# Kernel optimization log

Measured on AMD Instinct MI355X. Metric: run time of the kernel, lower is better.

Reference implementation:

```python
import jax, jax.numpy as jnp
import numpy as np

NEG_BIG = -9e15
LRELU_SLOPE = 0.2  # alpha

N = 8192
IN_F = 256
OUT_F = 128


def setup_inputs() -> dict:
    key = jax.random.key(0)
    k1, k2, k3, k4 = jax.random.split(key, 4)
    inputs = jax.random.normal(k1, (N, IN_F), dtype=jnp.float32)
    adj = jax.random.randint(k2, (N, N), 0, 2, dtype=jnp.int32)
    # xavier_uniform with gain=1.414
    gain = 1.414
    bW = gain * np.sqrt(6.0 / (IN_F + OUT_F))
    W = jax.random.uniform(k3, (IN_F, OUT_F), minval=-bW, maxval=bW, dtype=jnp.float32)
    ba = gain * np.sqrt(6.0 / (2 * OUT_F + 1))
    a = jax.random.uniform(k4, (2 * OUT_F, 1), minval=-ba, maxval=ba, dtype=jnp.float32)
    return {"inputs": inputs, "adj": adj, "W": W, "a": a}


def reference(inputs, adj, W, a):
    # h: [N, F']
    h = inputs @ W
    # a^T [h_i || h_j] = h_i . a[:F'] + h_j . a[F':]  -- avoids the O(N^2 * 2F') concat
    a1 = a[:OUT_F, 0]   # [F']
    a2 = a[OUT_F:, 0]   # [F']
    s1 = h @ a1         # [N]
    s2 = h @ a2         # [N]
    e = s1[:, None] + s2[None, :]                      # [N, N]
    e = jnp.where(e >= 0, e, LRELU_SLOPE * e)          # LeakyReLU(alpha)
    scores = jnp.where(adj > 0, e, jnp.float32(NEG_BIG))
    attention = jax.nn.softmax(scores, axis=1)         # row softmax; dropout p=0
    h_prime = attention @ h                            # [N, F']
    return jax.nn.elu(h_prime)                         # concat=True -> elu
```

## Files before the change

### kernel.cpp

```cpp
#include <hip/hip_runtime.h>
#include <hip/hip_bf16.h>

#define NN   8192
#define INF_ 256
#define OUTF 128
#define SLOPE 0.2f
#define NCH  2
#define CHJ  1024
#define NT_  16
#define NP_  16

typedef float f32x4  __attribute__((ext_vector_type(4)));
typedef float f32x16 __attribute__((ext_vector_type(16)));
typedef short bf16x8 __attribute__((ext_vector_type(8)));
typedef int   i32x4  __attribute__((ext_vector_type(4)));
typedef unsigned int u32;
typedef unsigned short u16;
typedef u16 u16x2 __attribute__((ext_vector_type(2)));

__device__ __forceinline__ u16 f2bf(float f) {
  return __builtin_bit_cast(u16, __float2bfloat16(f));
}


__global__ __launch_bounds__(256) void gat_k1(
    const float* __restrict__ X, const float* __restrict__ W,
    const float* __restrict__ a, u16* __restrict__ hbF,
    float* __restrict__ s1, float* __restrict__ s2) {
  __shared__ float xs[16 * INF_];
  const int t = threadIdx.x;
  const int r0 = blockIdx.x * 16;
  {
    const f32x4* src = (const f32x4*)(X + (size_t)r0 * INF_);
    f32x4* dst = (f32x4*)xs;
#pragma unroll
    for (int i = 0; i < 4; i++) dst[t + 256 * i] = src[t + 256 * i];
  }
  __syncthreads();
  const int cg = t & 31;
  const int rg = t >> 5;
  float acc[2][4];
#pragma unroll
  for (int i = 0; i < 2; i++)
#pragma unroll
    for (int j = 0; j < 4; j++) acc[i][j] = 0.f;

  for (int k = 0; k < INF_; k += 4) {
    f32x4 xv[2];
#pragma unroll
    for (int i = 0; i < 2; i++) xv[i] = *(const f32x4*)&xs[(rg * 2 + i) * INF_ + k];
#pragma unroll
    for (int kk = 0; kk < 4; kk++) {
      f32x4 wv = *(const f32x4*)&W[(k + kk) * OUTF + cg * 4];
#pragma unroll
      for (int i = 0; i < 2; i++)
#pragma unroll
        for (int j = 0; j < 4; j++) acc[i][j] = fmaf(xv[i][kk], wv[j], acc[i][j]);
    }
  }

  f32x4 a1v = *(const f32x4*)&a[cg * 4];
  f32x4 a2v = *(const f32x4*)&a[OUTF + cg * 4];
  float p1[2], p2[2];
#pragma unroll
  for (int i = 0; i < 2; i++) {
    p1[i] = acc[i][0] * a1v[0] + acc[i][1] * a1v[1] + acc[i][2] * a1v[2] + acc[i][3] * a1v[3];
    p2[i] = acc[i][0] * a2v[0] + acc[i][1] * a2v[1] + acc[i][2] * a2v[2] + acc[i][3] * a2v[3];
  }
#pragma unroll
  for (int m = 1; m < 32; m <<= 1) {
#pragma unroll
    for (int i = 0; i < 2; i++) {
      p1[i] += __shfl_xor(p1[i], m);
      p2[i] += __shfl_xor(p2[i], m);
    }
  }
  if (cg == 0) {
#pragma unroll
    for (int i = 0; i < 2; i++) {
      s1[r0 + rg * 2 + i] = p1[i];
      s2[r0 + rg * 2 + i] = p2[i];
    }
  }

  const int R0 = r0 + rg * 2;
  const int cc = R0 >> 10;
  const int rest = R0 & 1023;
  const int pr = rest >> 7;
  const int tt = (rest >> 3) & 15;
  const int e0 = R0 & 7;
  const int w_ = pr >> 1;
  const int g_ = pr & 1;
  const int n  = (cc * 16 + tt) * 4 + w_;
#pragma unroll
  for (int j = 0; j < 4; j++) {
    const int C = cg * 4 + j;
    u16x2 pk = {f2bf(acc[0][j]), f2bf(acc[1][j])};
    *(u16x2*)(hbF + ((size_t)(n * 4 + (C >> 5)) * 64 + g_ * 32 + (C & 31)) * 8 + e0) = pk;
  }
}

__global__ __launch_bounds__(256) void gat_k2(const float* __restrict__ s2,
                                              float* __restrict__ bmax,
                                              float* __restrict__ E1,
                                              float* __restrict__ E2) {
  __shared__ float sm[4];
  const int t = threadIdx.x;
  const int i = blockIdx.x * 256 + t;
  f32x4 v = ((const f32x4*)s2)[i];
  f32x4 e1, e2;
  float m = -1e30f;
#pragma unroll
  for (int k = 0; k < 4; k++) {
    m = fmaxf(m, v[k]);
    e1[k] = __expf(v[k]);
    e2[k] = __expf(SLOPE * v[k]);
  }
  ((f32x4*)E1)[i] = e1;
  ((f32x4*)E2)[i] = e2;
#pragma unroll
  for (int k = 1; k < 64; k <<= 1) m = fmaxf(m, __shfl_xor(m, k));
  if ((t & 63) == 0) sm[t >> 6] = m;
  __syncthreads();
  if (t == 0)
    bmax[blockIdx.x] = fmaxf(fmaxf(sm[0], sm[1]), fmaxf(sm[2], sm[3]));
}

__device__ __forceinline__ void st16(float* dst, const f32x16& A, int g) {
#pragma unroll
  for (int r = 0; r < 16; r++) {
    const int dr = (r & 3) + 8 * (r >> 2) + 4 * g;
    dst[dr * 128] = A[r];
  }
}
__device__ __forceinline__ void ad16(float* dst, const f32x16& A, int g) {
#pragma unroll
  for (int r = 0; r < 16; r++) {
    const int dr = (r & 3) + 8 * (r >> 2) + 4 * g;
    dst[dr * 128] += A[r];
  }
}

__global__ __launch_bounds__(256, 4) void gat_k3(
    const int* __restrict__ adj, const u16* __restrict__ hbF,
    const float* __restrict__ s1g, const float* __restrict__ E1,
    const float* __restrict__ E2, const float* __restrict__ bmax,
    float* __restrict__ part, float* __restrict__ dpart) {
  __shared__ unsigned char mb[2][4096];
  __shared__ float lred[4096];
  __shared__ float dred[128];
  const int t = threadIdx.x;
  const int w = t >> 6;
  const int l = t & 63;
  const int rb = blockIdx.x >> 2;
  const int jq = blockIdx.x & 3;
  const int r0 = rb * 32;
  const int row = l & 31;
  const int g = l >> 5;
  const int pr = 2 * w + g;

  float s2m = bmax[0];
#pragma unroll
  for (int k = 1; k < 8; k++) s2m = fmaxf(s2m, bmax[k]);
  const float s1r = s1g[r0 + row];
  float Mi = s1r + s2m;
  Mi = fmaxf(Mi, SLOPE * Mi);
  const float A = __expf(s1r - Mi);
  const float B = __expf(SLOPE * s1r - Mi);

  const int srow = t >> 3;
  const int cl = t & 7;
  const int* gsrc = adj + (size_t)(r0 + srow) * NN + jq * (NCH * CHJ) + cl * 8;

  i32x4 sA0, sA1, sB0, sB1;
#define LOADP(S0, S1, C, P)                        \
  {                                                \
    const int* p_ = gsrc + (C) * CHJ + (P) * 64;   \
    S0 = *(const i32x4*)(p_);                      \
    S1 = *(const i32x4*)(p_ + 4);                  \
  }
#define PACKP(S0, S1, P, NB)                                                 \
  {                                                                          \
    const int idx_ = (P)*8 + cl;                                             \
    const int pr_ = idx_ >> 4;                                               \
    const int tt_ = idx_ & 15;                                               \
    unsigned b_ = 0;                                                         \
    _Pragma("unroll") for (int e_ = 0; e_ < 4; e_++) {                       \
      b_ |= (S0[e_] > 0 ? 1u : 0u) << e_;                                    \
      b_ |= (S1[e_] > 0 ? 1u : 0u) << (e_ + 4);                              \
    }                                                                        \
    mb[NB][srow * 128 + ((pr_ ^ (srow & 7)) << 4) + tt_] = (unsigned char)b_;\
  }

  f32x16 acc0 = 0.f, acc1 = 0.f, acc2 = 0.f, acc3 = 0.f;
  float dsum = 0.f;

#define COMPUTE(CC, TT, BMV)                                                   \
  {                                                                            \
    const unsigned bl_ =                                                       \
        ((unsigned)(BMV)[(TT) >> 2] >> (((TT)&3) * 8)) & 0xffu;                \
    const int n0 = ((CC)*16 + (TT)) * 4 + w;                                   \
    const u16* q0 = hbF + (size_t)n0 * 2048 + l * 8;                           \
    bf16x8 b0 = *(const bf16x8*)(q0);                                          \
    bf16x8 b1 = *(const bf16x8*)(q0 + 512);                                    \
    bf16x8 b2 = *(const bf16x8*)(q0 + 1024);                                   \
    bf16x8 b3 = *(const bf16x8*)(q0 + 1536);                                   \
    const int j0 = (CC)*CHJ + pr * 128 + (TT)*8;                               \
    f32x4 u0 = *(const f32x4*)(E1 + j0);                                       \
    f32x4 u1 = *(const f32x4*)(E1 + j0 + 4);                                   \
    f32x4 v0 = *(const f32x4*)(E2 + j0);                                       \
    f32x4 v1 = *(const f32x4*)(E2 + j0 + 4);                                   \
    u32 aw[4];                                                                 \
    _Pragma("unroll") for (int e = 0; e < 8; e += 2) {                         \
      const float x0 = (e < 4) ? u0[e & 3] : u1[e & 3];                        \
      const float x1 = (e < 4) ? u0[(e + 1) & 3] : u1[(e + 1) & 3];            \
      const float y0 = (e < 4) ? v0[e & 3] : v1[e & 3];                        \
      const float y1 = (e < 4) ? v0[(e + 1) & 3] : v1[(e + 1) & 3];            \
      float pa = fmaxf(A * x0, B * y0);                                        \
      float pb = fmaxf(A * x1, B * y1);                                        \
      pa = (bl_ & (1u << e)) ? pa : 0.f;                                       \
      pb = (bl_ & (1u << (e + 1))) ? pb : 0.f;                                 \
      dsum += pa + pb;                                                         \
      aw[e >> 1] = __builtin_amdgcn_perm(                                      \
          __builtin_bit_cast(u32, pb) + 0x8000u,                               \
          __builtin_bit_cast(u32, pa) + 0x8000u, 0x07060302u);                 \
    }                                                                          \
    const bf16x8 af = __builtin_bit_cast(                                      \
        bf16x8, (i32x4){(int)aw[0], (int)aw[1], (int)aw[2], (int)aw[3]});      \
    acc0 = __builtin_amdgcn_mfma_f32_32x32x16_bf16(af, b0, acc0, 0, 0, 0);     \
    acc1 = __builtin_amdgcn_mfma_f32_32x32x16_bf16(af, b1, acc1, 0, 0, 0);     \
    acc2 = __builtin_amdgcn_mfma_f32_32x32x16_bf16(af, b2, acc2, 0, 0, 0);     \
    acc3 = __builtin_amdgcn_mfma_f32_32x32x16_bf16(af, b3, acc3, 0, 0, 0);     \
  }

  LOADP(sA0, sA1, 0, 0);
  LOADP(sB0, sB1, 0, 1);
#pragma unroll
  for (int p = 2; p < NP_; p += 2) {
    PACKP(sA0, sA1, p - 2, 0);
    LOADP(sA0, sA1, 0, p);
    PACKP(sB0, sB1, p - 1, 0);
    LOADP(sB0, sB1, 0, p + 1);
  }
  PACKP(sA0, sA1, 14, 0);
  PACKP(sB0, sB1, 15, 0);
  __syncthreads();

  for (int c = 0; c < NCH; c++) {
    const int cb = c & 1, nb = cb ^ 1;
    const int cc = jq * NCH + c;
    const i32x4 bmv =
        *(const i32x4*)&mb[cb][row * 128 + ((pr ^ (row & 7)) << 4)];
    const bool more = (c + 1 < NCH);

    for (int K = 0; K < NT_; K++) {
      if (more) {
        if ((K & 1) == 0) {
          if (K >= 2) PACKP(sA0, sA1, K - 2, nb);
          LOADP(sA0, sA1, c + 1, K);
        } else {
          if (K >= 2) PACKP(sB0, sB1, K - 2, nb);
          LOADP(sB0, sB1, c + 1, K);
        }
      }
      COMPUTE(cc, K, bmv);
    }
    if (more) {
      PACKP(sA0, sA1, 14, nb);
      PACKP(sB0, sB1, 15, nb);
    }
    __syncthreads();
  }

  dsum += __shfl_xor(dsum, 32);
  if (l < 32) dred[w * 32 + l] = dsum;

  const int colw = l & 31;
  if (w == 0) {
    st16(&lred[0 * 32 + colw], acc0, g);
    st16(&lred[1 * 32 + colw], acc1, g);
    st16(&lred[2 * 32 + colw], acc2, g);
    st16(&lred[3 * 32 + colw], acc3, g);
  }
  __syncthreads();
  if (w == 1) {
    ad16(&lred[0 * 32 + colw], acc0, g);
    ad16(&lred[1 * 32 + colw], acc1, g);
    ad16(&lred[2 * 32 + colw], acc2, g);
    ad16(&lred[3 * 32 + colw], acc3, g);
  }
  __syncthreads();
  if (w == 2) {
    ad16(&lred[0 * 32 + colw], acc0, g);
    ad16(&lred[1 * 32 + colw], acc1, g);
    ad16(&lred[2 * 32 + colw], acc2, g);
    ad16(&lred[3 * 32 + colw], acc3, g);
  }
  __syncthreads();
  if (w == 3) {
    ad16(&lred[0 * 32 + colw], acc0, g);
    ad16(&lred[1 * 32 + colw], acc1, g);
    ad16(&lred[2 * 32 + colw], acc2, g);
    ad16(&lred[3 * 32 + colw], acc3, g);
  }
  __syncthreads();

  if (t < 32) {
    float d = dred[t] + dred[32 + t] + dred[64 + t] + dred[96 + t];
    dpart[jq * NN + r0 + t] = d;
  }
  const int flat = t * 16;
  float* pp = part + (size_t)jq * (NN * OUTF) + (size_t)r0 * OUTF + flat;
#pragma unroll
  for (int i = 0; i < 4; i++)
    *(f32x4*)(pp + 4 * i) = *(f32x4*)&lred[flat + 4 * i];
}

__global__ __launch_bounds__(256) void gat_k4(
    const float* __restrict__ part, const float* __restrict__ dpart,
    float* __restrict__ out) {
  const int idx = blockIdx.x * 256 + threadIdx.x;
  const int e4 = idx * 4;
  const int i = e4 >> 7;
  f32x4 p = {0.f, 0.f, 0.f, 0.f};
  float d = 0.f;
#pragma unroll
  for (int jq = 0; jq < 4; jq++) {
    p += *(const f32x4*)&part[(size_t)jq * (NN * OUTF) + e4];
    d += dpart[jq * NN + i];
  }
  d = fmaxf(d, 1e-30f);
  f32x4 r;
#pragma unroll
  for (int k = 0; k < 4; k++) {
    float v = p[k] / d;
    r[k] = (v > 0.f) ? v : expm1f(v);
  }
  *(f32x4*)&out[e4] = r;
}

extern "C" void kernel_launch(void* const* d_in, const int* in_sizes, int n_in,
                              void* d_out, int out_size, void* d_ws, size_t ws_size,
                              hipStream_t stream) {
  (void)in_sizes; (void)n_in; (void)out_size; (void)ws_size;
  const float* X  = (const float*)d_in[0];
  const int*  adj = (const int*)d_in[1];
  const float* W  = (const float*)d_in[2];
  const float* a  = (const float*)d_in[3];
  float* out = (float*)d_out;

  char* ws = (char*)d_ws;
  u16*   hbF   = (u16*)ws;
  float* s1    = (float*)(ws + (2u << 20));
  float* s2    = (float*)(ws + (2u << 20) + (32u << 10));
  float* bmax  = (float*)(ws + (2u << 20) + (64u << 10));
  float* E1    = (float*)(ws + (2u << 20) + (128u << 10));
  float* E2    = (float*)(ws + (2u << 20) + (160u << 10));
  float* dpart = (float*)(ws + (2u << 20) + (192u << 10));
  float* part  = (float*)(ws + (4u << 20));

  gat_k1<<<NN / 16, 256, 0, stream>>>(X, W, a, hbF, s1, s2);
  gat_k2<<<8, 256, 0, stream>>>(s2, bmax, E1, E2);
  gat_k3<<<256 * 4, 256, 0, stream>>>(adj, hbF, s1, E1, E2, bmax, part, dpart);
  gat_k4<<<(NN * OUTF / 4) / 256, 256, 0, stream>>>(part, dpart, out);
}
```

Measured before the change: 128.2 us.

## Split attention kernel into producer and consumer warps with two-way column split

The main attention kernel now runs 512 threads per block. Four producer waves load adjacency rows and pack them into bitmasks in shared memory, while four consumer waves run the MFMA accumulation on the previous chunk. Each block now covers half of the columns (four chunks) instead of a quarter, so there are fewer partial sums to write and the final reduction reads two partials instead of four. In exchange, block count drops to 512 and the consumer waves no longer hide adjacency loads within their own instruction stream, so overlap depends on the two wave groups running concurrently.

```diff
diff --git a/kernel.cpp b/kernel.cpp
--- a/kernel.cpp
+++ b/kernel.cpp
@@ -5,7 +5,7 @@
 #define INF_ 256
 #define OUTF 128
 #define SLOPE 0.2f
-#define NCH  2
+#define NCH  4
 #define CHJ  1024
 #define NT_  16
 #define NP_  16
@@ -141,7 +141,7 @@
   }
 }
 
-__global__ __launch_bounds__(256, 4) void gat_k3(
+__global__ __launch_bounds__(512, 4) void gat_k3(
     const int* __restrict__ adj, const u16* __restrict__ hbF,
     const float* __restrict__ s1g, const float* __restrict__ E1,
     const float* __restrict__ E2, const float* __restrict__ bmax,
@@ -152,12 +152,13 @@
   const int t = threadIdx.x;
   const int w = t >> 6;
   const int l = t & 63;
-  const int rb = blockIdx.x >> 2;
-  const int jq = blockIdx.x & 3;
+  const bool isProd = (w >= 4);
+  const int rb = blockIdx.x >> 1;
+  const int jh = blockIdx.x & 1;
   const int r0 = rb * 32;
   const int row = l & 31;
   const int g = l >> 5;
-  const int pr = 2 * w + g;
+  const int pr = 2 * (w & 3) + g;
 
   float s2m = bmax[0];
 #pragma unroll
@@ -168,9 +169,10 @@
   const float A = __expf(s1r - Mi);
   const float B = __expf(SLOPE * s1r - Mi);
 
-  const int srow = t >> 3;
-  const int cl = t & 7;
-  const int* gsrc = adj + (size_t)(r0 + srow) * NN + jq * (NCH * CHJ) + cl * 8;
+  const int pt = t - 256;
+  const int srow = (pt & 255) >> 3;
+  const int cl = pt & 7;
+  const int* gsrc = adj + (size_t)(r0 + srow) * NN + jh * (NCH * CHJ) + cl * 8;
 
   i32x4 sA0, sA1, sB0, sB1;
 #define LOADP(S0, S1, C, P)                        \
@@ -191,6 +193,19 @@
     }                                                                        \
     mb[NB][srow * 128 + ((pr_ ^ (srow & 7)) << 4) + tt_] = (unsigned char)b_;\
   }
+#define STAGE_CHUNK(C, NB)                   \
+  {                                          \
+    LOADP(sA0, sA1, (C), 0);                 \
+    LOADP(sB0, sB1, (C), 1);                 \
+    _Pragma("unroll") for (int p = 2; p < NP_; p += 2) { \
+      PACKP(sA0, sA1, p - 2, (NB));          \
+      LOADP(sA0, sA1, (C), p);               \
+      PACKP(sB0, sB1, p - 1, (NB));          \
+      LOADP(sB0, sB1, (C), p + 1);           \
+    }                                        \
+    PACKP(sA0, sA1, 14, (NB));               \
+    PACKP(sB0, sB1, 15, (NB));               \
+  }
 
   f32x16 acc0 = 0.f, acc1 = 0.f, acc2 = 0.f, acc3 = 0.f;
   float dsum = 0.f;
@@ -199,7 +214,7 @@
   {                                                                            \
     const unsigned bl_ =                                                       \
         ((unsigned)(BMV)[(TT) >> 2] >> (((TT)&3) * 8)) & 0xffu;                \
-    const int n0 = ((CC)*16 + (TT)) * 4 + w;                                   \
+    const int n0 = ((CC)*16 + (TT)) * 4 + (w & 3);                             \
     const u16* q0 = hbF + (size_t)n0 * 2048 + l * 8;                           \
     bf16x8 b0 = *(const bf16x8*)(q0);                                          \
     bf16x8 b1 = *(const bf16x8*)(q0 + 512);                                    \
@@ -233,47 +248,23 @@
     acc3 = __builtin_amdgcn_mfma_f32_32x32x16_bf16(af, b3, acc3, 0, 0, 0);     \
   }
 
-  LOADP(sA0, sA1, 0, 0);
-  LOADP(sB0, sB1, 0, 1);
-#pragma unroll
-  for (int p = 2; p < NP_; p += 2) {
-    PACKP(sA0, sA1, p - 2, 0);
-    LOADP(sA0, sA1, 0, p);
-    PACKP(sB0, sB1, p - 1, 0);
-    LOADP(sB0, sB1, 0, p + 1);
-  }
-  PACKP(sA0, sA1, 14, 0);
-  PACKP(sB0, sB1, 15, 0);
+  if (isProd) STAGE_CHUNK(0, 0);
   __syncthreads();
 
   for (int c = 0; c < NCH; c++) {
-    const int cb = c & 1, nb = cb ^ 1;
-    const int cc = jq * NCH + c;
-    const i32x4 bmv =
-        *(const i32x4*)&mb[cb][row * 128 + ((pr ^ (row & 7)) << 4)];
-    const bool more = (c + 1 < NCH);
-
-    for (int K = 0; K < NT_; K++) {
-      if (more) {
-        if ((K & 1) == 0) {
-          if (K >= 2) PACKP(sA0, sA1, K - 2, nb);
-          LOADP(sA0, sA1, c + 1, K);
-        } else {
-          if (K >= 2) PACKP(sB0, sB1, K - 2, nb);
-          LOADP(sB0, sB1, c + 1, K);
-        }
-      }
-      COMPUTE(cc, K, bmv);
-    }
-    if (more) {
-      PACKP(sA0, sA1, 14, nb);
-      PACKP(sB0, sB1, 15, nb);
+    if (!isProd) {
+      const int cc = jh * NCH + c;
+      const i32x4 bmv =
+          *(const i32x4*)&mb[c & 1][row * 128 + ((pr ^ (row & 7)) << 4)];
+      for (int K = 0; K < NT_; K++) COMPUTE(cc, K, bmv);
+    } else if (c + 1 < NCH) {
+      STAGE_CHUNK(c + 1, (c + 1) & 1);
     }
     __syncthreads();
   }
 
   dsum += __shfl_xor(dsum, 32);
-  if (l < 32) dred[w * 32 + l] = dsum;
+  if (!isProd && l < 32) dred[(w & 3) * 32 + l] = dsum;
 
   const int colw = l & 31;
   if (w == 0) {
@@ -307,13 +298,15 @@
 
   if (t < 32) {
     float d = dred[t] + dred[32 + t] + dred[64 + t] + dred[96 + t];
-    dpart[jq * NN + r0 + t] = d;
-  }
-  const int flat = t * 16;
-  float* pp = part + (size_t)jq * (NN * OUTF) + (size_t)r0 * OUTF + flat;
-#pragma unroll
-  for (int i = 0; i < 4; i++)
-    *(f32x4*)(pp + 4 * i) = *(f32x4*)&lred[flat + 4 * i];
+    dpart[jh * NN + r0 + t] = d;
+  }
+  if (t < 256) {
+    const int flat = t * 16;
+    float* pp = part + (size_t)jh * (NN * OUTF) + (size_t)r0 * OUTF + flat;
+#pragma unroll
+    for (int i = 0; i < 4; i++)
+      *(f32x4*)(pp + 4 * i) = *(f32x4*)&lred[flat + 4 * i];
+  }
 }
 
 __global__ __launch_bounds__(256) void gat_k4(
@@ -322,13 +315,9 @@
   const int idx = blockIdx.x * 256 + threadIdx.x;
   const int e4 = idx * 4;
   const int i = e4 >> 7;
-  f32x4 p = {0.f, 0.f, 0.f, 0.f};
-  float d = 0.f;
-#pragma unroll
-  for (int jq = 0; jq < 4; jq++) {
-    p += *(const f32x4*)&part[(size_t)jq * (NN * OUTF) + e4];
-    d += dpart[jq * NN + i];
-  }
+  f32x4 p = *(const f32x4*)&part[e4];
+  p += *(const f32x4*)&part[(size_t)(NN * OUTF) + e4];
+  float d = dpart[i] + dpart[NN + i];
   d = fmaxf(d, 1e-30f);
   f32x4 r;
 #pragma unroll
@@ -361,6 +350,6 @@
 
   gat_k1<<<NN / 16, 256, 0, stream>>>(X, W, a, hbF, s1, s2);
   gat_k2<<<8, 256, 0, stream>>>(s2, bmax, E1, E2);
-  gat_k3<<<256 * 4, 256, 0, stream>>>(adj, hbF, s1, E1, E2, bmax, part, dpart);
+  gat_k3<<<512, 512, 0, stream>>>(adj, hbF, s1, E1, E2, bmax, part, dpart);
   gat_k4<<<(NN * OUTF / 4) / 256, 256, 0, stream>>>(part, dpart, out);
 }
```

Result: slower. 160.7 us (+25.4%).
